# Performance work log

Hardware: AMD Instinct MI355X
Metric: run time of the kernel (lower is better)

The kernel has to match this reference:

```python
import jax, jax.numpy as jnp
import numpy as np

B, S, D, H = 8, 1024, 768, 12
DH = D // H  # per-head dim = 64


def setup_inputs() -> dict:
    key = jax.random.key(0)
    ks = jax.random.split(key, 9)
    scale = 1.0 / np.sqrt(D)
    x = jax.random.normal(ks[0], (B, S, D), dtype=jnp.float32)
    # Per-head projection weights stacked over the head axis [H, D, DH]
    Wq = jax.random.normal(ks[1], (H, D, DH), dtype=jnp.float32) * scale
    bq = jax.random.normal(ks[2], (H, DH), dtype=jnp.float32) * 0.02
    Wk = jax.random.normal(ks[3], (H, D, DH), dtype=jnp.float32) * scale
    bk = jax.random.normal(ks[4], (H, DH), dtype=jnp.float32) * 0.02
    Wv = jax.random.normal(ks[5], (H, D, DH), dtype=jnp.float32) * scale
    bv = jax.random.normal(ks[6], (H, DH), dtype=jnp.float32) * 0.02
    Wo = jax.random.normal(ks[7], (D, D), dtype=jnp.float32) * scale
    bo = jax.random.normal(ks[8], (D,), dtype=jnp.float32) * 0.02
    return {"x": x, "Wq": Wq, "bq": bq, "Wk": Wk, "bk": bk,
            "Wv": Wv, "bv": bv, "Wo": Wo, "bo": bo}


def reference(x, Wq, bq, Wk, bk, Wv, bv, Wo, bo):
    # Batched equivalent of the per-head Python loop: each head has its own
    # Q/K/V linear projections (weights stacked on the head axis).
    q = jnp.einsum('bsd,hde->bhse', x, Wq) + bq[None, :, None, :]
    k = jnp.einsum('bsd,hde->bhse', x, Wk) + bk[None, :, None, :]
    v = jnp.einsum('bsd,hde->bhse', x, Wv) + bv[None, :, None, :]
    scores = jnp.einsum('bhse,bhte->bhst', q, k) / jnp.sqrt(jnp.float32(DH))
    attn = jax.nn.softmax(scores, axis=-1)
    out = jnp.einsum('bhst,bhte->bhse', attn, v)  # [B,H,S,DH]
    # concat heads on last dim -> [B,S,H*DH] = [B,S,D]
    out = out.transpose(0, 2, 1, 3).reshape(B, S, D)
    return out @ Wo.T + bo
```

## Files before the change

kernel.cpp:

```cpp
#include <hip/hip_runtime.h>
#include <hip/hip_bf16.h>


typedef unsigned short u16;
typedef unsigned int u32;
typedef __attribute__((ext_vector_type(8))) short bf16x8;
typedef __attribute__((ext_vector_type(8))) unsigned short u16x8;
typedef __attribute__((ext_vector_type(4))) float f32x4;
typedef __attribute__((ext_vector_type(4))) u32 u32x4;

typedef __attribute__((address_space(1))) const u32* gas_u32;
typedef __attribute__((address_space(3))) u32* las_u32;

#define DEVI __device__ __forceinline__

DEVI u16 f2bf(float f) {
  union { float f; u32 u; } v; v.f = f;
  u32 r = v.u + 0x7fffu + ((v.u >> 16) & 1u);
  return (u16)(r >> 16);
}

DEVI void gll16(const void* g, void* l) {
  __builtin_amdgcn_global_load_lds((gas_u32)g, (las_u32)l, 16, 0, 0);
}

DEVI f32x4 mfma16(bf16x8 a, bf16x8 b, f32x4 c) {
  return __builtin_amdgcn_mfma_f32_16x16x32_bf16(a, b, c, 0, 0, 0);
}

DEVI u32 cvtpk(float lo, float hi) {
  u32 r;
  asm("v_cvt_pk_bf16_f32 %0, %1, %2" : "=v"(r) : "v"(lo), "v"(hi));
  return r;
}

__global__ __launch_bounds__(256) void k_prep(const float* __restrict__ x,
                                              u16* __restrict__ xb,
                                              const float* __restrict__ Wo,
                                              u16* __restrict__ Wob,
                                              const float* __restrict__ Wq,
                                              const float* __restrict__ Wk,
                                              const float* __restrict__ Wv,
                                              u16* __restrict__ Wtb) {
  __shared__ u16 T[64][65];
  const int blk = blockIdx.x;
  const int tid = threadIdx.x;
  if (blk < 6720) {
    const float* in; u16* out; int idx;
    if (blk < 6144) { in = x;  out = xb;  idx = blk * 256 + tid; }
    else            { in = Wo; out = Wob; idx = (blk - 6144) * 256 + tid; }
    float4 v = ((const float4*)in)[idx];
    ushort4 o;
    o.x = f2bf(v.x); o.y = f2bf(v.y); o.z = f2bf(v.z); o.w = f2bf(v.w);
    ((ushort4*)out)[idx] = o;
    return;
  }
  const int blk2 = blk - 6720;
  const int th = blk2 / 12;
  const int k0 = (blk2 % 12) * 64;
  const float* W = (th < 12) ? Wq : (th < 24) ? Wk : Wv;
  const int h = th % 12;
  W += (size_t)h * 768 * 64;
  const int row = tid >> 2, c = tid & 3;
  const float* src = W + (size_t)(k0 + row) * 64 + c * 16;
#pragma unroll
  for (int j = 0; j < 4; ++j) {
    float4 v = ((const float4*)src)[j];
    T[row][c * 16 + j * 4 + 0] = f2bf(v.x);
    T[row][c * 16 + j * 4 + 1] = f2bf(v.y);
    T[row][c * 16 + j * 4 + 2] = f2bf(v.z);
    T[row][c * 16 + j * 4 + 3] = f2bf(v.w);
  }
  __syncthreads();
  const int e = tid >> 2;
  u16* dst = Wtb + ((size_t)th * 64 + e) * 768 + k0 + c * 16;
  alignas(16) u16 tmp[16];
#pragma unroll
  for (int j = 0; j < 16; ++j) tmp[j] = T[c * 16 + j][e];
  *(u16x8*)(dst)     = *(const u16x8*)(tmp);
  *(u16x8*)(dst + 8) = *(const u16x8*)(tmp + 8);
}

__global__ __launch_bounds__(256) void k_gemmQKV(const u16* __restrict__ Ab,
                                                 const u16* __restrict__ Wtb,
                                                 const float* __restrict__ bq,
                                                 const float* __restrict__ bk,
                                                 const float* __restrict__ bv,
                                                 u16* __restrict__ Qb,
                                                 u16* __restrict__ VTb) {
  __shared__ u16 smem[2][12288];
  const int tid = threadIdx.x;
  const int w = tid >> 6, lane = tid & 63, lq = lane & 15, g = lane >> 4;
  const int wm = w >> 1, wn = w & 1;
  const int m0 = blockIdx.x * 128;
  const int pn = blockIdx.y;
  const u16* Arows = Ab + (size_t)m0 * 768;
  const u16* Brows = Wtb + (size_t)pn * 64 * 768;

  f32x4 acc[4][2];
#pragma unroll
  for (int mf = 0; mf < 4; ++mf)
#pragma unroll
    for (int nf = 0; nf < 2; ++nf) acc[mf][nf] = (f32x4){0.f, 0.f, 0.f, 0.f};

#define QSTAGE(buf, kt_)                                                         \
  {                                                                              \
    const int kb_ = (kt_) * 64;                                                  \
    _Pragma("unroll")                                                            \
    for (int i = 0; i < 4; ++i) {                                                \
      int c = w * 4 + i;                                                         \
      int id = c * 64 + lane;                                                    \
      int row = id >> 3, cb = id & 7;                                            \
      gll16(Arows + (size_t)row * 768 + kb_ + ((cb ^ (row & 7)) << 3),           \
            &smem[buf][c * 512]);                                                \
    }                                                                            \
    _Pragma("unroll")                                                            \
    for (int i = 0; i < 2; ++i) {                                                \
      int c = w * 2 + i;                                                         \
      int id = c * 64 + lane;                                                    \
      int row = id >> 3, cb = id & 7;                                            \
      gll16(Brows + (size_t)row * 768 + kb_ + ((cb ^ (row & 7)) << 3),           \
            &smem[buf][8192 + c * 512]);                                         \
    }                                                                            \
  }

#define QCOMP(buf)                                                               \
  {                                                                              \
    const u16* As_ = &smem[buf][0];                                              \
    const u16* Bs_ = &smem[buf][8192];                                           \
    _Pragma("unroll")                                                            \
    for (int kk = 0; kk < 2; ++kk) {                                             \
      bf16x8 a[4], b[2];                                                         \
      _Pragma("unroll")                                                          \
      for (int mf = 0; mf < 4; ++mf) {                                           \
        int row = wm * 64 + mf * 16 + lq;                                        \
        a[mf] = *(const bf16x8*)(As_ + row * 64 +                                \
                                 (((kk * 64 + g * 16) ^ ((row & 7) << 4)) >> 1)); \
      }                                                                          \
      _Pragma("unroll")                                                          \
      for (int nf = 0; nf < 2; ++nf) {                                           \
        int row = wn * 32 + nf * 16 + lq;                                        \
        b[nf] = *(const bf16x8*)(Bs_ + row * 64 +                                \
                                 (((kk * 64 + g * 16) ^ ((row & 7) << 4)) >> 1)); \
      }                                                                          \
      _Pragma("unroll")                                                          \
      for (int mf = 0; mf < 4; ++mf)                                             \
        _Pragma("unroll")                                                        \
        for (int nf = 0; nf < 2; ++nf)                                           \
          acc[mf][nf] = mfma16(a[mf], b[nf], acc[mf][nf]);                       \
    }                                                                            \
  }

  QSTAGE(0, 0)
  asm volatile("s_waitcnt vmcnt(0)" ::: "memory");
  __syncthreads();
  for (int it = 0; it < 6; ++it) {
    const int kt = it * 2;
    QSTAGE(1, kt + 1)
    QCOMP(0)
    asm volatile("s_waitcnt vmcnt(0)" ::: "memory");
    __syncthreads();
    if (it < 5) QSTAGE(0, kt + 2)
    QCOMP(1)
    if (it < 5) {
      asm volatile("s_waitcnt vmcnt(0)" ::: "memory");
      __syncthreads();
    }
  }
#undef QSTAGE
#undef QCOMP

  const int sel = pn / 12;
  const int ph  = pn % 12;
  const int b = m0 >> 10;
  if (sel == 2) {
    __syncthreads();
    u16* Ct = &smem[0][0];
#pragma unroll
    for (int nf = 0; nf < 2; ++nf) {
      const int e = wn * 32 + nf * 16 + lq;
      const float bi = bv[ph * 64 + e];
#pragma unroll
      for (int mf = 0; mf < 4; ++mf)
#pragma unroll
        for (int r = 0; r < 4; ++r) {
          int sl = wm * 64 + mf * 16 + 4 * g + r;
          Ct[e * 136 + sl] = f2bf(acc[mf][nf][r] + bi);
        }
    }
    __syncthreads();
    const int er = tid >> 2, cc = tid & 3;
    u16* dst = VTb + ((size_t)(b * 12 + ph) * 64 + er) * 1024 + (m0 & 1023) + cc * 32;
#pragma unroll
    for (int i = 0; i < 4; ++i)
      *(u16x8*)(dst + i * 8) = *(const u16x8*)(Ct + er * 136 + cc * 32 + i * 8);
  } else {
    u16* out = Qb + (size_t)sel * 6291456;
    const float qs = sel ? 1.0f : 0.18033688f;
    const float* bp = sel ? bk : bq;
#pragma unroll
    for (int nf = 0; nf < 2; ++nf) {
      const int e = wn * 32 + nf * 16 + lq;
      const float bi = bp[ph * 64 + e];
#pragma unroll
      for (int mf = 0; mf < 4; ++mf)
#pragma unroll
        for (int r = 0; r < 4; ++r) {
          int s = (m0 & 1023) + wm * 64 + mf * 16 + 4 * g + r;
          out[((size_t)(b * 12 + ph) * 1024 + s) * 64 + e] = f2bf((acc[mf][nf][r] + bi) * qs);
        }
    }
  }
}

__global__ __launch_bounds__(256) void k_gemmO(const u16* __restrict__ Ab,
                                               const u16* __restrict__ Bb,
                                               const float* __restrict__ bias,
                                               float* __restrict__ out) {
  __shared__ u16 smem[2][12288];
  const int tid = threadIdx.x;
  const int w = tid >> 6, lane = tid & 63, lq = lane & 15, g = lane >> 4;
  const int wm = w >> 1, wn = w & 1;
  const int m0 = blockIdx.x * 128;
  const int pn = blockIdx.y;
  const u16* Arows = Ab + (size_t)m0 * 768;
  const u16* Brows = Bb + (size_t)pn * 64 * 768;

  f32x4 acc[4][2];
#pragma unroll
  for (int mf = 0; mf < 4; ++mf)
#pragma unroll
    for (int nf = 0; nf < 2; ++nf) acc[mf][nf] = (f32x4){0.f, 0.f, 0.f, 0.f};

#define OSTAGE(buf, kt_)                                                         \
  {                                                                              \
    const int kb_ = (kt_) * 64;                                                  \
    _Pragma("unroll")                                                            \
    for (int i = 0; i < 4; ++i) {                                                \
      int c = w * 4 + i;                                                         \
      int id = c * 64 + lane;                                                    \
      int row = id >> 3, cb = id & 7;                                            \
      gll16(Arows + (size_t)row * 768 + kb_ + ((cb ^ (row & 7)) << 3),           \
            &smem[buf][c * 512]);                                                \
    }                                                                            \
    _Pragma("unroll")                                                            \
    for (int i = 0; i < 2; ++i) {                                                \
      int c = w * 2 + i;                                                         \
      int id = c * 64 + lane;                                                    \
      int row = id >> 3, cb = id & 7;                                            \
      gll16(Brows + (size_t)row * 768 + kb_ + ((cb ^ (row & 7)) << 3),           \
            &smem[buf][8192 + c * 512]);                                         \
    }                                                                            \
  }

#define OCOMP(buf)                                                               \
  {                                                                              \
    const u16* As_ = &smem[buf][0];                                              \
    const u16* Bs_ = &smem[buf][8192];                                           \
    _Pragma("unroll")                                                            \
    for (int kk = 0; kk < 2; ++kk) {                                             \
      bf16x8 a[4], b[2];                                                         \
      _Pragma("unroll")                                                          \
      for (int mf = 0; mf < 4; ++mf) {                                           \
        int row = wm * 64 + mf * 16 + lq;                                        \
        a[mf] = *(const bf16x8*)(As_ + row * 64 +                                \
                                 (((kk * 64 + g * 16) ^ ((row & 7) << 4)) >> 1)); \
      }                                                                          \
      _Pragma("unroll")                                                          \
      for (int nf = 0; nf < 2; ++nf) {                                           \
        int row = wn * 32 + nf * 16 + lq;                                        \
        b[nf] = *(const bf16x8*)(Bs_ + row * 64 +                                \
                                 (((kk * 64 + g * 16) ^ ((row & 7) << 4)) >> 1)); \
      }                                                                          \
      _Pragma("unroll")                                                          \
      for (int mf = 0; mf < 4; ++mf)                                             \
        _Pragma("unroll")                                                        \
        for (int nf = 0; nf < 2; ++nf)                                           \
          acc[mf][nf] = mfma16(a[mf], b[nf], acc[mf][nf]);                       \
    }                                                                            \
  }

  OSTAGE(0, 0)
  asm volatile("s_waitcnt vmcnt(0)" ::: "memory");
  __syncthreads();
  for (int it = 0; it < 6; ++it) {
    const int kt = it * 2;
    OSTAGE(1, kt + 1)
    OCOMP(0)
    asm volatile("s_waitcnt vmcnt(0)" ::: "memory");
    __syncthreads();
    if (it < 5) OSTAGE(0, kt + 2)
    OCOMP(1)
    if (it < 5) {
      asm volatile("s_waitcnt vmcnt(0)" ::: "memory");
      __syncthreads();
    }
  }
#undef OSTAGE
#undef OCOMP

#pragma unroll
  for (int nf = 0; nf < 2; ++nf) {
    const int n = pn * 64 + wn * 32 + nf * 16 + lq;
    const float bi = bias[n];
#pragma unroll
    for (int mf = 0; mf < 4; ++mf)
#pragma unroll
      for (int r = 0; r < 4; ++r) {
        int m = m0 + wm * 64 + mf * 16 + 4 * g + r;
        out[(size_t)m * 768 + n] = acc[mf][nf][r] + bi;
      }
  }
}

__global__ __launch_bounds__(512) void k_attn(const u16* __restrict__ Qb,
                                              const u16* __restrict__ Kb,
                                              const u16* __restrict__ VTb,
                                              u16* __restrict__ AO) {
  __shared__ u16 Ksm[2][4096];
  __shared__ u16 Vsm[2][4096];
  const int tid = threadIdx.x;
  const int w = tid >> 6, lane = tid & 63, lq = lane & 15, g = lane >> 4;
  const int bh = blockIdx.x, b = bh / 12, h = bh % 12;
  const int q0 = blockIdx.y * 128 + w * 16;
  const u16* Qw = Qb + ((size_t)bh * 1024 + q0) * 64;
  const u16* Kp = Kb + (size_t)bh * 65536;
  const u16* Vp = VTb + (size_t)bh * 65536;
  const bool gsel = (g & 1);

  bf16x8 qf[2];
#pragma unroll
  for (int kk = 0; kk < 2; ++kk)
    qf[kk] = *(const bf16x8*)(Qw + lq * 64 + kk * 32 + g * 8);

  f32x4 o[4];
#pragma unroll
  for (int ef = 0; ef < 4; ++ef) o[ef] = (f32x4){0.f, 0.f, 0.f, 0.f};
  float l_ = 0.f;

#define STAGE(buf, kt_)                                                          \
  {                                                                              \
    const int kb_ = (kt_) * 64;                                                  \
    const int id = w * 64 + lane;                                                \
    const int row = id >> 3, cb = id & 7;                                        \
    const int sb = cb ^ (row & 7);                                               \
    const int tb = (sb & 4) | ((sb & 1) << 1) | ((sb >> 1) & 1);                 \
    gll16(Kp + (size_t)(kb_ + row) * 64 + (sb << 3), &Ksm[buf][w * 512]);        \
    gll16(Vp + (size_t)row * 1024 + kb_ + (tb << 3), &Vsm[buf][w * 512]);        \
  }

#define TILE(buf)                                                                \
  {                                                                              \
    f32x4 s[4];                                                                  \
    _Pragma("unroll")                                                            \
    for (int kf = 0; kf < 4; ++kf) s[kf] = (f32x4){0.f, 0.f, 0.f, 0.f};          \
    __builtin_amdgcn_s_setprio(1);                                               \
    _Pragma("unroll")                                                            \
    for (int kf = 0; kf < 4; ++kf) {                                             \
      const int row = kf * 16 + lq;                                              \
      _Pragma("unroll")                                                          \
      for (int kk = 0; kk < 2; ++kk) {                                           \
        bf16x8 kfr = *(const bf16x8*)(&Ksm[buf][0] + row * 64 +                  \
                                      (((kk * 64 + g * 16) ^ ((row & 7) << 4)) >> 1)); \
        s[kf] = mfma16(kfr, qf[kk], s[kf]);                                      \
      }                                                                          \
    }                                                                            \
    __builtin_amdgcn_s_setprio(0);                                               \
    float sm = 0.f;                                                              \
    _Pragma("unroll")                                                            \
    for (int kf = 0; kf < 4; ++kf)                                               \
      _Pragma("unroll")                                                          \
      for (int r = 0; r < 4; ++r) {                                              \
        float p = __builtin_amdgcn_exp2f(s[kf][r]);                              \
        s[kf][r] = p;                                                            \
        sm += p;                                                                 \
      }                                                                          \
    l_ += sm;                                                                    \
    u32 D[4][2];                                                                 \
    _Pragma("unroll")                                                            \
    for (int kf = 0; kf < 4; ++kf) {                                             \
      D[kf][0] = cvtpk(s[kf][0], s[kf][1]);                                      \
      D[kf][1] = cvtpk(s[kf][2], s[kf][3]);                                      \
    }                                                                            \
    _Pragma("unroll")                                                            \
    for (int kk = 0; kk < 2; ++kk) {                                             \
      const int kk2 = kk * 2;                                                    \
      u32 sa0 = gsel ? D[kk2][0] : D[kk2 + 1][0];                                \
      u32 sa1 = gsel ? D[kk2][1] : D[kk2 + 1][1];                                \
      u32 xa0 = __shfl_xor(sa0, 16), xa1 = __shfl_xor(sa1, 16);                  \
      u32x4 t = { gsel ? xa0 : D[kk2][0],                                        \
                  gsel ? xa1 : D[kk2][1],                                        \
                  gsel ? D[kk2 + 1][0] : xa0,                                    \
                  gsel ? D[kk2 + 1][1] : xa1 };                                  \
      bf16x8 pb = __builtin_bit_cast(bf16x8, t);                                 \
      __builtin_amdgcn_s_setprio(1);                                             \
      _Pragma("unroll")                                                          \
      for (int ef = 0; ef < 4; ++ef) {                                           \
        const int row = ef * 16 + lq;                                            \
        bf16x8 vf = *(const bf16x8*)(&Vsm[buf][0] + row * 64 +                   \
                                     (((kk * 64 + g * 16) ^ ((row & 7) << 4)) >> 1)); \
        o[ef] = mfma16(vf, pb, o[ef]);                                           \
      }                                                                          \
      __builtin_amdgcn_s_setprio(0);                                             \
    }                                                                            \
  }

  STAGE(0, 0)
  asm volatile("s_waitcnt vmcnt(0)" ::: "memory");
  __syncthreads();

  for (int it = 0; it < 8; ++it) {
    const int kt = it * 2;
    STAGE(1, kt + 1)
    TILE(0)
    asm volatile("s_waitcnt vmcnt(0)" ::: "memory");
    __syncthreads();
    if (it < 7) STAGE(0, kt + 2)
    TILE(1)
    if (it < 7) {
      asm volatile("s_waitcnt vmcnt(0)" ::: "memory");
      __syncthreads();
    }
  }

  l_ += __shfl_xor(l_, 16);
  l_ += __shfl_xor(l_, 32);

  const float inv = 1.0f / l_;
  u16* dst = AO + ((size_t)(b * 1024 + q0 + lq)) * 768 + h * 64 + g * 4;
#pragma unroll
  for (int ef = 0; ef < 4; ++ef) {
    ushort4 t;
    t.x = f2bf(o[ef][0] * inv);
    t.y = f2bf(o[ef][1] * inv);
    t.z = f2bf(o[ef][2] * inv);
    t.w = f2bf(o[ef][3] * inv);
    *(ushort4*)(dst + ef * 16) = t;
  }
#undef STAGE
#undef TILE
}

extern "C" void kernel_launch(void* const* d_in, const int* in_sizes, int n_in,
                              void* d_out, int out_size, void* d_ws, size_t ws_size,
                              hipStream_t stream) {
  (void)in_sizes; (void)n_in; (void)out_size; (void)ws_size;
  const float* x  = (const float*)d_in[0];
  const float* Wq = (const float*)d_in[1];
  const float* bq = (const float*)d_in[2];
  const float* Wk = (const float*)d_in[3];
  const float* bk = (const float*)d_in[4];
  const float* Wv = (const float*)d_in[5];
  const float* bv = (const float*)d_in[6];
  const float* Wo = (const float*)d_in[7];
  const float* bo = (const float*)d_in[8];

  char* ws = (char*)d_ws;
  u16* xb  = (u16*)(ws);
  u16* Wtb = (u16*)(ws + 12582912);
  u16* Wob = (u16*)(ws + 12582912 + 3538944);
  u16* Qb  = (u16*)(ws + 12582912 + 3538944 + 1179648);
  u16* Kb  = Qb + (size_t)96 * 1024 * 64;
  u16* VTb = Kb + (size_t)96 * 1024 * 64;
  u16* AO  = xb;

  k_prep<<<7152, 256, 0, stream>>>(x, xb, Wo, Wob, Wq, Wk, Wv, Wtb);

  k_gemmQKV<<<dim3(64, 36), 256, 0, stream>>>(xb, Wtb, bq, bk, bv, Qb, VTb);

  k_attn<<<dim3(96, 8), 512, 0, stream>>>(Qb, Kb, VTb, AO);

  k_gemmO<<<dim3(64, 12), 256, 0, stream>>>(AO, Wob, bo, (float*)d_out);
}
```

Measured before the change: 106.7 us.

## Fuse Q, K, V projections per head into one block to reuse A tile

Result: faster. 99.54 us, median of 2 (-6.7%).

```diff
diff --git a/kernel.cpp b/kernel.cpp
--- a/kernel.cpp
+++ b/kernel.cpp
@@ -81,123 +81,88 @@
   *(u16x8*)(dst + 8) = *(const u16x8*)(tmp + 8);
 }
 
-__global__ __launch_bounds__(256) void k_gemmQKV(const u16* __restrict__ Ab,
-                                                 const u16* __restrict__ Wtb,
-                                                 const float* __restrict__ bq,
-                                                 const float* __restrict__ bk,
-                                                 const float* __restrict__ bv,
-                                                 u16* __restrict__ Qb,
-                                                 u16* __restrict__ VTb) {
-  __shared__ u16 smem[2][12288];
+__global__ __launch_bounds__(256, 3) void k_gemmQKV(const u16* __restrict__ Ab,
+                                                    const u16* __restrict__ Wtb,
+                                                    const float* __restrict__ bq,
+                                                    const float* __restrict__ bk,
+                                                    const float* __restrict__ bv,
+                                                    u16* __restrict__ Qb,
+                                                    u16* __restrict__ VTb) {
+  __shared__ u16 smem[20480];
   const int tid = threadIdx.x;
   const int w = tid >> 6, lane = tid & 63, lq = lane & 15, g = lane >> 4;
   const int wm = w >> 1, wn = w & 1;
   const int m0 = blockIdx.x * 128;
-  const int pn = blockIdx.y;
+  const int ph = blockIdx.y;
   const u16* Arows = Ab + (size_t)m0 * 768;
-  const u16* Brows = Wtb + (size_t)pn * 64 * 768;
-
-  f32x4 acc[4][2];
-#pragma unroll
-  for (int mf = 0; mf < 4; ++mf)
-#pragma unroll
-    for (int nf = 0; nf < 2; ++nf) acc[mf][nf] = (f32x4){0.f, 0.f, 0.f, 0.f};
-
-#define QSTAGE(buf, kt_)                                                         \
-  {                                                                              \
-    const int kb_ = (kt_) * 64;                                                  \
-    _Pragma("unroll")                                                            \
-    for (int i = 0; i < 4; ++i) {                                                \
-      int c = w * 4 + i;                                                         \
-      int id = c * 64 + lane;                                                    \
-      int row = id >> 3, cb = id & 7;                                            \
-      gll16(Arows + (size_t)row * 768 + kb_ + ((cb ^ (row & 7)) << 3),           \
-            &smem[buf][c * 512]);                                                \
-    }                                                                            \
-    _Pragma("unroll")                                                            \
-    for (int i = 0; i < 2; ++i) {                                                \
-      int c = w * 2 + i;                                                         \
-      int id = c * 64 + lane;                                                    \
-      int row = id >> 3, cb = id & 7;                                            \
-      gll16(Brows + (size_t)row * 768 + kb_ + ((cb ^ (row & 7)) << 3),           \
-            &smem[buf][8192 + c * 512]);                                         \
-    }                                                                            \
-  }
-
-#define QCOMP(buf)                                                               \
-  {                                                                              \
-    const u16* As_ = &smem[buf][0];                                              \
-    const u16* Bs_ = &smem[buf][8192];                                           \
-    _Pragma("unroll")                                                            \
-    for (int kk = 0; kk < 2; ++kk) {                                             \
-      bf16x8 a[4], b[2];                                                         \
-      _Pragma("unroll")                                                          \
-      for (int mf = 0; mf < 4; ++mf) {                                           \
-        int row = wm * 64 + mf * 16 + lq;                                        \
-        a[mf] = *(const bf16x8*)(As_ + row * 64 +                                \
-                                 (((kk * 64 + g * 16) ^ ((row & 7) << 4)) >> 1)); \
-      }                                                                          \
-      _Pragma("unroll")                                                          \
-      for (int nf = 0; nf < 2; ++nf) {                                           \
-        int row = wn * 32 + nf * 16 + lq;                                        \
-        b[nf] = *(const bf16x8*)(Bs_ + row * 64 +                                \
-                                 (((kk * 64 + g * 16) ^ ((row & 7) << 4)) >> 1)); \
-      }                                                                          \
-      _Pragma("unroll")                                                          \
-      for (int mf = 0; mf < 4; ++mf)                                             \
-        _Pragma("unroll")                                                        \
-        for (int nf = 0; nf < 2; ++nf)                                           \
-          acc[mf][nf] = mfma16(a[mf], b[nf], acc[mf][nf]);                       \
-    }                                                                            \
-  }
-
-  QSTAGE(0, 0)
-  asm volatile("s_waitcnt vmcnt(0)" ::: "memory");
-  __syncthreads();
-  for (int it = 0; it < 6; ++it) {
-    const int kt = it * 2;
-    QSTAGE(1, kt + 1)
-    QCOMP(0)
+  const u16* B0 = Wtb + (size_t)ph * 64 * 768;
+  const u16* B1 = Wtb + (size_t)(12 + ph) * 64 * 768;
+  const u16* B2 = Wtb + (size_t)(24 + ph) * 64 * 768;
+
+  f32x4 acc[3][4][2];
+#pragma unroll
+  for (int s = 0; s < 3; ++s)
+#pragma unroll
+    for (int mf = 0; mf < 4; ++mf)
+#pragma unroll
+      for (int nf = 0; nf < 2; ++nf) acc[s][mf][nf] = (f32x4){0.f, 0.f, 0.f, 0.f};
+
+  for (int kt = 0; kt < 12; ++kt) {
+    const int kb = kt * 64;
+#pragma unroll
+    for (int i = 0; i < 4; ++i) {
+      int c = w * 4 + i;
+      int id = c * 64 + lane;
+      int row = id >> 3, cb = id & 7;
+      gll16(Arows + (size_t)row * 768 + kb + ((cb ^ (row & 7)) << 3), &smem[c * 512]);
+    }
+#pragma unroll
+    for (int i = 0; i < 2; ++i) {
+      int c = w * 2 + i;
+      int id = c * 64 + lane;
+      int row = id >> 3, cb = id & 7;
+      int sw = (cb ^ (row & 7)) << 3;
+      size_t off = (size_t)row * 768 + kb + sw;
+      gll16(B0 + off, &smem[8192 + c * 512]);
+      gll16(B1 + off, &smem[12288 + c * 512]);
+      gll16(B2 + off, &smem[16384 + c * 512]);
+    }
     asm volatile("s_waitcnt vmcnt(0)" ::: "memory");
     __syncthreads();
-    if (it < 5) QSTAGE(0, kt + 2)
-    QCOMP(1)
-    if (it < 5) {
-      asm volatile("s_waitcnt vmcnt(0)" ::: "memory");
-      __syncthreads();
-    }
-  }
-#undef QSTAGE
-#undef QCOMP
-
-  const int sel = pn / 12;
-  const int ph  = pn % 12;
+#pragma unroll
+    for (int kk = 0; kk < 2; ++kk) {
+      bf16x8 a[4];
+#pragma unroll
+      for (int mf = 0; mf < 4; ++mf) {
+        int row = wm * 64 + mf * 16 + lq;
+        a[mf] = *(const bf16x8*)(&smem[0] + row * 64 +
+                                 (((kk * 64 + g * 16) ^ ((row & 7) << 4)) >> 1));
+      }
+#pragma unroll
+      for (int s = 0; s < 3; ++s) {
+        bf16x8 b[2];
+#pragma unroll
+        for (int nf = 0; nf < 2; ++nf) {
+          int row = wn * 32 + nf * 16 + lq;
+          b[nf] = *(const bf16x8*)(&smem[8192 + s * 4096] + row * 64 +
+                                   (((kk * 64 + g * 16) ^ ((row & 7) << 4)) >> 1));
+        }
+#pragma unroll
+        for (int mf = 0; mf < 4; ++mf)
+#pragma unroll
+          for (int nf = 0; nf < 2; ++nf)
+            acc[s][mf][nf] = mfma16(a[mf], b[nf], acc[s][mf][nf]);
+      }
+    }
+    if (kt < 11) __syncthreads();
+  }
+
   const int b = m0 >> 10;
-  if (sel == 2) {
-    __syncthreads();
-    u16* Ct = &smem[0][0];
-#pragma unroll
-    for (int nf = 0; nf < 2; ++nf) {
-      const int e = wn * 32 + nf * 16 + lq;
-      const float bi = bv[ph * 64 + e];
-#pragma unroll
-      for (int mf = 0; mf < 4; ++mf)
-#pragma unroll
-        for (int r = 0; r < 4; ++r) {
-          int sl = wm * 64 + mf * 16 + 4 * g + r;
-          Ct[e * 136 + sl] = f2bf(acc[mf][nf][r] + bi);
-        }
-    }
-    __syncthreads();
-    const int er = tid >> 2, cc = tid & 3;
-    u16* dst = VTb + ((size_t)(b * 12 + ph) * 64 + er) * 1024 + (m0 & 1023) + cc * 32;
-#pragma unroll
-    for (int i = 0; i < 4; ++i)
-      *(u16x8*)(dst + i * 8) = *(const u16x8*)(Ct + er * 136 + cc * 32 + i * 8);
-  } else {
-    u16* out = Qb + (size_t)sel * 6291456;
-    const float qs = sel ? 1.0f : 0.18033688f;
-    const float* bp = sel ? bk : bq;
+#pragma unroll
+  for (int s = 0; s < 2; ++s) {
+    u16* out = Qb + (size_t)s * 6291456;
+    const float qs = s ? 1.0f : 0.18033688f;
+    const float* bp = s ? bk : bq;
 #pragma unroll
     for (int nf = 0; nf < 2; ++nf) {
       const int e = wn * 32 + nf * 16 + lq;
@@ -206,11 +171,32 @@
       for (int mf = 0; mf < 4; ++mf)
 #pragma unroll
         for (int r = 0; r < 4; ++r) {
-          int s = (m0 & 1023) + wm * 64 + mf * 16 + 4 * g + r;
-          out[((size_t)(b * 12 + ph) * 1024 + s) * 64 + e] = f2bf((acc[mf][nf][r] + bi) * qs);
+          int srow = (m0 & 1023) + wm * 64 + mf * 16 + 4 * g + r;
+          out[((size_t)(b * 12 + ph) * 1024 + srow) * 64 + e] =
+              f2bf((acc[s][mf][nf][r] + bi) * qs);
         }
     }
   }
+  __syncthreads();
+  u16* Ct = &smem[0];
+#pragma unroll
+  for (int nf = 0; nf < 2; ++nf) {
+    const int e = wn * 32 + nf * 16 + lq;
+    const float bi = bv[ph * 64 + e];
+#pragma unroll
+    for (int mf = 0; mf < 4; ++mf)
+#pragma unroll
+      for (int r = 0; r < 4; ++r) {
+        int sl = wm * 64 + mf * 16 + 4 * g + r;
+        Ct[e * 136 + sl] = f2bf(acc[2][mf][nf][r] + bi);
+      }
+  }
+  __syncthreads();
+  const int er = tid >> 2, cc = tid & 3;
+  u16* dst = VTb + ((size_t)(b * 12 + ph) * 64 + er) * 1024 + (m0 & 1023) + cc * 32;
+#pragma unroll
+  for (int i = 0; i < 4; ++i)
+    *(u16x8*)(dst + i * 8) = *(const u16x8*)(Ct + er * 136 + cc * 32 + i * 8);
 }
 
 __global__ __launch_bounds__(256) void k_gemmO(const u16* __restrict__ Ab,
@@ -466,7 +452,7 @@
 
   k_prep<<<7152, 256, 0, stream>>>(x, xb, Wo, Wob, Wq, Wk, Wv, Wtb);
 
-  k_gemmQKV<<<dim3(64, 36), 256, 0, stream>>>(xb, Wtb, bq, bk, bv, Qb, VTb);
+  k_gemmQKV<<<dim3(64, 12), 256, 0, stream>>>(xb, Wtb, bq, bk, bv, Qb, VTb);
 
   k_attn<<<dim3(96, 8), 512, 0, stream>>>(Qb, Kb, VTb, AO);
 
```
